# Optimization experiments

Measured on AMD Instinct MI355X. Metric: run time of the kernel, lower is better.

Reference implementation:

```python
import jax, jax.numpy as jnp
import numpy as np

N_E = 1024
E_DIM = 64
BETA = 0.25
DECAY = 0.99
EPSILON = 1e-5


def setup_inputs() -> dict:
    key = jax.random.key(0)
    k1, k2, k3 = jax.random.split(key, 3)
    z = jax.random.normal(k1, (32, E_DIM, 32, 32), dtype=jnp.float32)
    # codebook initialized uniform(-1/n_e, 1/n_e) as in the torch module
    emb_w = jax.random.uniform(k2, (N_E, E_DIM), minval=-1.0 / N_E, maxval=1.0 / N_E, dtype=jnp.float32)
    ema_cluster_size = jnp.ones((N_E,), dtype=jnp.float32)
    ema_w = jax.random.uniform(k3, (N_E, E_DIM), minval=-1.0 / N_E, maxval=1.0 / N_E, dtype=jnp.float32)
    return {"z": z, "emb_w": emb_w, "ema_cluster_size": ema_cluster_size, "ema_w": ema_w}


def reference(z, emb_w, ema_cluster_size, ema_w):
    B, C, H, W = z.shape  # C == E_DIM
    zf = jnp.transpose(z, (0, 2, 3, 1)).reshape(-1, E_DIM)  # [N, e_dim]
    N = zf.shape[0]

    # squared-distance via ||z||^2 + ||e||^2 - 2 z.e (same expansion as torch code)
    d = (jnp.sum(zf * zf, axis=1, keepdims=True)
         + jnp.sum(emb_w * emb_w, axis=1)
         - 2.0 * zf @ emb_w.T)  # [N, n_e]
    idx = jnp.argmin(d, axis=1)  # [N]

    min_encodings = jax.nn.one_hot(idx, N_E, dtype=jnp.float32)  # [N, n_e]
    # cluster stats via scatter-add (equivalent to one-hot matmuls, cheaper)
    cluster_size = jax.ops.segment_sum(jnp.ones((N,), jnp.float32), idx, num_segments=N_E)
    sum_encodings = jax.ops.segment_sum(zf, idx, num_segments=N_E)  # [n_e, e_dim]

    # EMA update (training path, done before the z_q lookup as in torch)
    new_cs = DECAY * ema_cluster_size + (1.0 - DECAY) * cluster_size
    new_w = DECAY * ema_w + (1.0 - DECAY) * sum_encodings
    n = jnp.sum(new_cs)
    cs_norm = (new_cs + EPSILON) / (n + N_E * EPSILON) * n
    new_emb = new_w / cs_norm[:, None]  # updated codebook

    z_q = new_emb[idx].reshape(B, H, W, C).transpose(0, 3, 1, 2)  # [B,C,H,W]
    loss = BETA * jnp.mean((jax.lax.stop_gradient(z_q) - z) ** 2)
    z_q_st = z + jax.lax.stop_gradient(z_q - z)  # straight-through

    avg_probs = cluster_size / N
    perplexity = jnp.exp(-jnp.sum(avg_probs * jnp.log(avg_probs + 1e-10)))
    return loss, z_q_st, perplexity, min_encodings, idx
```

## Files before the change

kernel.cpp:

```cpp
#include <hip/hip_runtime.h>
#include <math.h>

#define NVEC 32768
#define NE   1024
#define ED   64
#define TOT  2097152
#define NCHUNK 8
#define CHUNK  128
#define MT     64

#define O_LOSS   0
#define O_ZQ     1
#define O_PERP   2097153
#define O_MINENC 2097154
#define O_IDX    35651586

#define W_PIDX   0
#define W_CS     32768
#define W_SUMENC 33792
#define W_NEWEMB 99328
#define W_LOSSP  164864

__global__ void __launch_bounds__(256, 3) k_dist(const float* __restrict__ z,
                                                 const float* __restrict__ emb,
                                                 int* __restrict__ fidx,
                                                 float* __restrict__ out) {
    __shared__ __align__(16) float s_a[64 * 64];
    __shared__ __align__(16) float s_b[64 * 132];
    __shared__ float s_esq[CHUNK];
    __shared__ float s_zsq[MT];
    __shared__ int sbi[MT];

    int tid = threadIdx.x;
    int n0 = blockIdx.x * MT;
    int b = n0 >> 10, hw0 = n0 & 1023;
    const float* zb = z + b * 65536 + hw0;

#pragma unroll
    for (int j = 0; j < 4; ++j) {
        int f4i = j * 256 + tid;
        int c = f4i >> 4, pos = (f4i & 15) * 4;
        float4 v = *(const float4*)(zb + (c << 10) + pos);
        v.x = __fmul_rn(2.0f, v.x);
        v.y = __fmul_rn(2.0f, v.y);
        v.z = __fmul_rn(2.0f, v.z);
        v.w = __fmul_rn(2.0f, v.w);
        *(float4*)(s_a + c * 64 + pos) = v;
    }
    __syncthreads();

    if (tid < MT) {
        float r[8];
#pragma unroll
        for (int j = 0; j < 8; ++j) {
            float v = s_a[j * 64 + tid];
            r[j] = __fmul_rn(v, v);
        }
#pragma unroll
        for (int i = 8; i < 64; i += 8)
#pragma unroll
            for (int j = 0; j < 8; ++j) {
                float v = s_a[(i + j) * 64 + tid];
                r[j] = __fadd_rn(r[j], __fmul_rn(v, v));
            }
        s_zsq[tid] = __fmul_rn(0.25f, __fadd_rn(
            __fadd_rn(__fadd_rn(r[0], r[1]), __fadd_rn(r[2], r[3])),
            __fadd_rn(__fadd_rn(r[4], r[5]), __fadd_rn(r[6], r[7]))));
    }
    __syncthreads();

    int mi = tid & 15, ki = tid >> 4;
    int mbase = mi * 4, kbase = ki * 8;
    float zs[4];
#pragma unroll
    for (int mu = 0; mu < 4; ++mu) zs[mu] = s_zsq[mbase + mu];

    float bd[4];
    int bix[4];
#pragma unroll
    for (int mu = 0; mu < 4; ++mu) { bd[mu] = 3.4e38f; bix[mu] = kbase; }

    for (int q = 0; q < NCHUNK; ++q) {
        int k0 = q * CHUNK;
        __syncthreads();
#pragma unroll
        for (int j = 0; j < 8; ++j) {
            int f4i = j * 256 + tid;
            int kl = f4i >> 4, c0 = (f4i & 15) * 4;
            float4 v = *(const float4*)(emb + (size_t)(k0 + kl) * ED + c0);
            s_b[(c0 + 0) * 132 + kl] = v.x;
            s_b[(c0 + 1) * 132 + kl] = v.y;
            s_b[(c0 + 2) * 132 + kl] = v.z;
            s_b[(c0 + 3) * 132 + kl] = v.w;
        }
        if (tid < CHUNK) {
            const float* ep = emb + (size_t)(k0 + tid) * ED;
            float r[8];
#pragma unroll
            for (int j = 0; j < 8; ++j) r[j] = __fmul_rn(ep[j], ep[j]);
#pragma unroll
            for (int i = 8; i < 64; i += 8)
#pragma unroll
                for (int j = 0; j < 8; ++j)
                    r[j] = __fadd_rn(r[j], __fmul_rn(ep[i + j], ep[i + j]));
            s_esq[tid] = __fadd_rn(
                __fadd_rn(__fadd_rn(r[0], r[1]), __fadd_rn(r[2], r[3])),
                __fadd_rn(__fadd_rn(r[4], r[5]), __fadd_rn(r[6], r[7])));
        }
        __syncthreads();

        float acc[4][8];
#pragma unroll
        for (int mu = 0; mu < 4; ++mu)
#pragma unroll
            for (int ku = 0; ku < 8; ++ku) acc[mu][ku] = 0.f;

#pragma unroll 4
        for (int c = 0; c < 64; ++c) {
            float4 av = *(const float4*)(s_a + c * 64 + mbase);
            float4 b0 = *(const float4*)(s_b + c * 132 + kbase);
            float4 b1 = *(const float4*)(s_b + c * 132 + kbase + 4);
#pragma unroll
            for (int mu = 0; mu < 4; ++mu) {
                float a = (&av.x)[mu];
                acc[mu][0] = __fmaf_rn(a, b0.x, acc[mu][0]);
                acc[mu][1] = __fmaf_rn(a, b0.y, acc[mu][1]);
                acc[mu][2] = __fmaf_rn(a, b0.z, acc[mu][2]);
                acc[mu][3] = __fmaf_rn(a, b0.w, acc[mu][3]);
                acc[mu][4] = __fmaf_rn(a, b1.x, acc[mu][4]);
                acc[mu][5] = __fmaf_rn(a, b1.y, acc[mu][5]);
                acc[mu][6] = __fmaf_rn(a, b1.z, acc[mu][6]);
                acc[mu][7] = __fmaf_rn(a, b1.w, acc[mu][7]);
            }
        }

#pragma unroll
        for (int mu = 0; mu < 4; ++mu)
#pragma unroll
            for (int ku = 0; ku < 8; ++ku) {
                float d = __fsub_rn(__fadd_rn(zs[mu], s_esq[kbase + ku]),
                                    acc[mu][ku]);
                if (d < bd[mu]) { bd[mu] = d; bix[mu] = k0 + kbase + ku; }
            }
    }

    __syncthreads();
    float* red_d = s_b;
    int* red_i = (int*)(s_b + 1024);
#pragma unroll
    for (int mu = 0; mu < 4; ++mu) {
        red_d[ki * 64 + mbase + mu] = bd[mu];
        red_i[ki * 64 + mbase + mu] = bix[mu];
    }
    __syncthreads();
    if (tid < MT) {
        float best = red_d[tid];
        int bi = red_i[tid];
#pragma unroll
        for (int q = 1; q < 16; ++q) {
            float d = red_d[q * 64 + tid];
            int i = red_i[q * 64 + tid];
            if (d < best || (d == best && i < bi)) { best = d; bi = i; }
        }
        fidx[n0 + tid] = bi;
        out[O_IDX + n0 + tid] = (float)bi;
        sbi[tid] = bi;
    }
    __syncthreads();
    int wave = tid >> 6, lane = tid & 63;
    size_t base = (size_t)O_MINENC + (size_t)n0 * NE;
    for (int r = wave; r < MT; r += 4) {
        int rbi = sbi[r];
        float* rp = out + base + (size_t)r * NE;
#pragma unroll
        for (int s = 0; s < 8; ++s) {
            int col = s * 128 + lane * 2;
            float2 v;
            v.x = (col == rbi) ? 1.0f : 0.0f;
            v.y = (col + 1 == rbi) ? 1.0f : 0.0f;
            *(float2*)(rp + col) = v;
        }
    }
}

__global__ void __launch_bounds__(256) k_sumenc(const int* __restrict__ idx,
                                                const float* __restrict__ z,
                                                float* __restrict__ cs,
                                                float* __restrict__ sumenc) {
    int k = blockIdx.x;
    int wave = threadIdx.x >> 6, lane = threadIdx.x & 63;
    float acc = 0.f;
    int cnt = 0;
    int base = wave * 8192;
    for (int it = 0; it < 128; ++it) {
        int n0 = base + it * 64;
        int idv = idx[n0 + lane];
        unsigned long long m = __ballot(idv == k);
        cnt += __popcll(m);
        while (m) {
            int bit = __ffsll((unsigned long long)m) - 1;
            m &= m - 1;
            int n = n0 + bit;
            int b = n >> 10, hw = n & 1023;
            acc = __fadd_rn(acc, z[b * 65536 + lane * 1024 + hw]);
        }
    }
    __shared__ float sacc[4][64];
    __shared__ int scnt[4];
    sacc[wave][lane] = acc;
    if (lane == 0) scnt[wave] = cnt;
    __syncthreads();
    if (wave == 0) {
        float t = __fadd_rn(__fadd_rn(sacc[0][lane], sacc[1][lane]),
                            __fadd_rn(sacc[2][lane], sacc[3][lane]));
        sumenc[k * ED + lane] = t;
        if (lane == 0) cs[k] = (float)(scnt[0] + scnt[1] + scnt[2] + scnt[3]);
    }
}

__global__ void __launch_bounds__(1024) k_ema(const float* __restrict__ ema_cs,
                                              const float* __restrict__ ema_w,
                                              const float* __restrict__ cs,
                                              const float* __restrict__ sumenc,
                                              float* __restrict__ newemb,
                                              float* __restrict__ out) {
    int k = threadIdx.x;
    float c = cs[k];
    float ncs = 0.99f * ema_cs[k] + (1.0f - 0.99f) * c;
    float p = c * (1.0f / (float)NVEC);
    float e = p * logf(p + 1e-10f);
    float rn_ = ncs, re_ = e;
#pragma unroll
    for (int o = 32; o > 0; o >>= 1) {
        rn_ += __shfl_down(rn_, o, 64);
        re_ += __shfl_down(re_, o, 64);
    }
    __shared__ float sn[16], se_[16];
    __shared__ float s_n;
    int wave = k >> 6, lane = k & 63;
    if (lane == 0) { sn[wave] = rn_; se_[wave] = re_; }
    __syncthreads();
    if (k == 0) {
        float tn = 0.f, te = 0.f;
#pragma unroll
        for (int w = 0; w < 16; ++w) { tn += sn[w]; te += se_[w]; }
        s_n = tn;
        out[O_PERP] = expf(-te);
    }
    __syncthreads();
    float nt = s_n;
    float csn = (ncs + 1e-5f) / (nt + 1024.0f * 1e-5f) * nt;
    __shared__ float s_csn[NE];
    s_csn[k] = csn;
    __syncthreads();
    for (int t = k; t < NE * ED; t += 1024) {
        float nw = 0.99f * ema_w[t] + (1.0f - 0.99f) * sumenc[t];
        newemb[t] = nw / s_csn[t >> 6];
    }
}

__global__ void __launch_bounds__(256) k_zq(const float* __restrict__ z,
                                            const int* __restrict__ idx,
                                            const float* __restrict__ newemb,
                                            float* __restrict__ out,
                                            float* __restrict__ lossp) {
    float local = 0.f;
#pragma unroll
    for (int i = 0; i < 4; ++i) {
        int t = blockIdx.x * 256 + threadIdx.x + i * 524288;
        int b = t >> 16, c = (t >> 10) & 63, hw = t & 1023;
        int n = (b << 10) | hw;
        float e = newemb[idx[n] * ED + c];
        float zv = z[t];
        float diff = e - zv;
        out[O_ZQ + t] = zv + diff;
        local = fmaf(diff, diff, local);
    }
#pragma unroll
    for (int o = 32; o > 0; o >>= 1) local += __shfl_down(local, o, 64);
    __shared__ float sp[4];
    int wave = threadIdx.x >> 6;
    if ((threadIdx.x & 63) == 0) sp[wave] = local;
    __syncthreads();
    if (threadIdx.x == 0)
        lossp[blockIdx.x] = (sp[0] + sp[1]) + (sp[2] + sp[3]);
}

__global__ void __launch_bounds__(256) k_fin(const float* __restrict__ lossp,
                                             float* __restrict__ out) {
    float v = 0.f;
#pragma unroll
    for (int i = 0; i < 8; ++i) v += lossp[i * 256 + threadIdx.x];
#pragma unroll
    for (int o = 32; o > 0; o >>= 1) v += __shfl_down(v, o, 64);
    __shared__ float sp[4];
    int wave = threadIdx.x >> 6;
    if ((threadIdx.x & 63) == 0) sp[wave] = v;
    __syncthreads();
    if (threadIdx.x == 0)
        out[O_LOSS] = 0.25f * (((sp[0] + sp[1]) + (sp[2] + sp[3])) * (1.0f / (float)TOT));
}

extern "C" void kernel_launch(void* const* d_in, const int* in_sizes, int n_in,
                              void* d_out, int out_size, void* d_ws, size_t ws_size,
                              hipStream_t stream) {
    const float* z      = (const float*)d_in[0];
    const float* emb    = (const float*)d_in[1];
    const float* ema_cs = (const float*)d_in[2];
    const float* ema_w  = (const float*)d_in[3];
    float* out = (float*)d_out;
    float* ws  = (float*)d_ws;

    k_dist<<<512, 256, 0, stream>>>(z, emb, (int*)(ws + W_PIDX), out);
    k_sumenc<<<NE, 256, 0, stream>>>((const int*)(ws + W_PIDX), z, ws + W_CS,
                                     ws + W_SUMENC);
    k_ema<<<1, 1024, 0, stream>>>(ema_cs, ema_w, ws + W_CS, ws + W_SUMENC,
                                  ws + W_NEWEMB, out);
    k_zq<<<2048, 256, 0, stream>>>(z, (const int*)(ws + W_PIDX), ws + W_NEWEMB, out,
                                   ws + W_LOSSP);
    k_fin<<<1, 256, 0, stream>>>(ws + W_LOSSP, out);
}
```

Before: 293.5 us.

## Swizzle codebook LDS layout and split one-hot write into aligned float4 kernel

Rotates the column placement of codebook entries in shared memory by an XOR-like swizzle so the transposed stores and float4 reads in the distance GEMM avoid bank conflicts. Moves the 128 MB one-hot output write out of the distance kernel into a separate kernel. That kernel uses 16-byte aligned float4 stores, offset by 2 because the one-hot region starts at a float offset that is not 16-byte aligned. This trades an extra launch and an extra read of the indices for wider, aligned stores and a lighter distance kernel.

```diff
diff --git a/kernel.cpp b/kernel.cpp
--- a/kernel.cpp
+++ b/kernel.cpp
@@ -29,7 +29,6 @@
     __shared__ __align__(16) float s_b[64 * 132];
     __shared__ float s_esq[CHUNK];
     __shared__ float s_zsq[MT];
-    __shared__ int sbi[MT];
 
     int tid = threadIdx.x;
     int n0 = blockIdx.x * MT;
@@ -86,12 +85,13 @@
 #pragma unroll
         for (int j = 0; j < 8; ++j) {
             int f4i = j * 256 + tid;
-            int kl = f4i >> 4, c0 = (f4i & 15) * 4;
-            float4 v = *(const float4*)(emb + (size_t)(k0 + kl) * ED + c0);
-            s_b[(c0 + 0) * 132 + kl] = v.x;
-            s_b[(c0 + 1) * 132 + kl] = v.y;
-            s_b[(c0 + 2) * 132 + kl] = v.z;
-            s_b[(c0 + 3) * 132 + kl] = v.w;
+            int kl = f4i >> 4, c4 = f4i & 15;
+            float4 v = *(const float4*)(emb + (size_t)(k0 + kl) * ED + c4 * 4);
+            int base = ((( kl >> 2) + c4) & 31) * 4 + (kl & 3);
+            s_b[(c4 * 4 + 0) * 132 + base] = v.x;
+            s_b[(c4 * 4 + 1) * 132 + base] = v.y;
+            s_b[(c4 * 4 + 2) * 132 + base] = v.z;
+            s_b[(c4 * 4 + 3) * 132 + base] = v.w;
         }
         if (tid < CHUNK) {
             const float* ep = emb + (size_t)(k0 + tid) * ED;
@@ -117,9 +117,10 @@
 
 #pragma unroll 4
         for (int c = 0; c < 64; ++c) {
+            int c4 = c >> 2;
             float4 av = *(const float4*)(s_a + c * 64 + mbase);
-            float4 b0 = *(const float4*)(s_b + c * 132 + kbase);
-            float4 b1 = *(const float4*)(s_b + c * 132 + kbase + 4);
+            float4 b0 = *(const float4*)(s_b + c * 132 + ((2 * ki + c4) & 31) * 4);
+            float4 b1 = *(const float4*)(s_b + c * 132 + ((2 * ki + 1 + c4) & 31) * 4);
 #pragma unroll
             for (int mu = 0; mu < 4; ++mu) {
                 float a = (&av.x)[mu];
@@ -164,21 +165,37 @@
         }
         fidx[n0 + tid] = bi;
         out[O_IDX + n0 + tid] = (float)bi;
-        sbi[tid] = bi;
-    }
-    __syncthreads();
-    int wave = tid >> 6, lane = tid & 63;
-    size_t base = (size_t)O_MINENC + (size_t)n0 * NE;
-    for (int r = wave; r < MT; r += 4) {
+    }
+}
+
+__global__ void __launch_bounds__(256) k_onehot(const int* __restrict__ idx,
+                                                float* __restrict__ out) {
+    __shared__ int sbi[16];
+    int r0 = blockIdx.x * 16;
+    if (threadIdx.x < 16) sbi[threadIdx.x] = idx[r0 + threadIdx.x];
+    __syncthreads();
+    int t = threadIdx.x;
+    for (int r = 0; r < 16; ++r) {
         int rbi = sbi[r];
-        float* rp = out + base + (size_t)r * NE;
-#pragma unroll
-        for (int s = 0; s < 8; ++s) {
-            int col = s * 128 + lane * 2;
-            float2 v;
+        float* rp = out + O_MINENC + (size_t)(r0 + r) * NE;
+        if (t < 254) {
+            int col = 2 + t * 4;
+            float4 v;
             v.x = (col == rbi) ? 1.0f : 0.0f;
             v.y = (col + 1 == rbi) ? 1.0f : 0.0f;
-            *(float2*)(rp + col) = v;
+            v.z = (col + 2 == rbi) ? 1.0f : 0.0f;
+            v.w = (col + 3 == rbi) ? 1.0f : 0.0f;
+            *(float4*)(rp + col) = v;
+        } else if (t == 254) {
+            float2 v;
+            v.x = (0 == rbi) ? 1.0f : 0.0f;
+            v.y = (1 == rbi) ? 1.0f : 0.0f;
+            *(float2*)(rp) = v;
+        } else {
+            float2 v;
+            v.x = (1022 == rbi) ? 1.0f : 0.0f;
+            v.y = (1023 == rbi) ? 1.0f : 0.0f;
+            *(float2*)(rp + 1022) = v;
         }
     }
 }
@@ -312,6 +329,7 @@
     float* ws  = (float*)d_ws;
 
     k_dist<<<512, 256, 0, stream>>>(z, emb, (int*)(ws + W_PIDX), out);
+    k_onehot<<<2048, 256, 0, stream>>>((const int*)(ws + W_PIDX), out);
     k_sumenc<<<NE, 256, 0, stream>>>((const int*)(ws + W_PIDX), z, ws + W_CS,
                                      ws + W_SUMENC);
     k_ema<<<1, 1024, 0, stream>>>(ema_cs, ema_w, ws + W_CS, ws + W_SUMENC,
```

Result: no change. 292.6 us (-0.3%).
